# Optimization experiments

Hardware: AMD Instinct MI355X
Metric: run time of the kernel (lower is better)

Reference implementation:

```python
import jax, jax.numpy as jnp
import numpy as np

B, S, D, H = 8, 1024, 1024, 16  # batch, seq (queries==keys), d_model, heads
DH = D // H


def setup_inputs() -> dict:
    key = jax.random.key(0)
    ks = jax.random.split(key, 7)
    return {
        "query": jax.random.normal(ks[0], (B, S, D), dtype=jnp.float32),
        "key": jax.random.normal(ks[1], (B, S, D), dtype=jnp.float32),
        "value": jax.random.normal(ks[2], (B, S, D), dtype=jnp.float32),
        "valid_len": jax.random.randint(ks[3], (B, S), 0, S, dtype=jnp.int32),
        "Wq": jax.random.normal(ks[4], (D, D), dtype=jnp.float32) / np.sqrt(D),
        "Wk": jax.random.normal(ks[5], (D, D), dtype=jnp.float32) / np.sqrt(D),
        "Wv": jax.random.normal(ks[6], (D, D), dtype=jnp.float32) / np.sqrt(D),
    }


def reference(query, key, value, valid_len, Wq, Wk, Wv):
    b, sq, _ = query.shape
    sk = key.shape[1]
    # projections (bias-free Linear), then split hidden into H contiguous chunks per head
    q = (query @ Wq).reshape(b, sq, H, DH)  # [B,Sq,H,dh]
    k = (key @ Wk).reshape(b, sk, H, DH)
    v = (value @ Wv).reshape(b, sk, H, DH)
    scale = 1.0 / jnp.sqrt(jnp.asarray(DH, dtype=q.dtype))
    scores = jnp.einsum("bqhd,bkhd->bhqk", q, k) * scale  # [B,H,Sq,Sk]
    # per-query mask (valid_len.dim()==2 path): key index < valid_len[b, q]
    col = jnp.arange(sk)
    mask = col[None, None, None, :] < valid_len[:, None, :, None]  # [B,1,Sq,Sk]
    scores = jnp.where(mask, scores, jnp.asarray(-1000.0, dtype=scores.dtype))
    prob = jax.nn.softmax(scores, axis=-1)
    out = jnp.einsum("bhqk,bkhd->bqhd", prob, v)  # [B,Sq,H,dh]
    return out.reshape(b, sq, D)
```

## Files before the change

### kernel.cpp

```cpp
#include <hip/hip_runtime.h>
#include <hip/hip_bf16.h>
#include <stdint.h>


#define B_  8
#define S_  1024
#define D_  1024
#define H_  16
#define DH_ 64

typedef short bf16x8 __attribute__((ext_vector_type(8)));
typedef float f32x4  __attribute__((ext_vector_type(4)));
typedef unsigned short u16;
typedef uint32_t u32;
typedef u16 u16x8 __attribute__((ext_vector_type(8)));
typedef u16 u16x4 __attribute__((ext_vector_type(4)));

#define MASKVAL  (-1442.6950408889634f)
#define QSCALE   (0.18033688011112042f)

union U4 { u32 u[4]; bf16x8 v; };

__device__ __forceinline__ u16 f2bf(float f) {
    union { float f; uint32_t u; } v; v.f = f;
    uint32_t u = v.u;
    return (u16)((u + 0x7FFFu + ((u >> 16) & 1u)) >> 16);
}

__device__ __forceinline__ u32 cvtpk(float lo, float hi) {
    u32 r;
    asm("v_cvt_pk_bf16_f32 %0, %1, %2" : "=v"(r) : "v"(lo), "v"(hi));
    return r;
}

__device__ __forceinline__ void gload16(const void* g, const void* l) {
    __builtin_amdgcn_global_load_lds(
        (const __attribute__((address_space(1))) void*)g,
        (__attribute__((address_space(3))) void*)l, 16, 0, 0);
}

__device__ __forceinline__ float xor32max(float v) {
    float a = v, b = v;
    asm volatile("" : "+v"(b));
    asm("v_permlane32_swap_b32 %0, %1" : "+v"(a), "+v"(b));
    return fmaxf(a, b);
}
__device__ __forceinline__ float xor32add(float v) {
    float a = v, b = v;
    asm volatile("" : "+v"(b));
    asm("v_permlane32_swap_b32 %0, %1" : "+v"(a), "+v"(b));
    return a + b;
}

__global__ void transpose_w3_kernel(const float* __restrict__ Wq, const float* __restrict__ Wk,
                                    const float* __restrict__ Wv, u16* __restrict__ Wts) {
    __shared__ u16 tile[32 * 33];
    const int z = blockIdx.z;
    const float* W = (z == 0) ? Wq : (z == 1) ? Wk : Wv;
    u16* Wt = Wts + (size_t)z * D_ * D_;
    int k0 = blockIdx.y * 32, n0 = blockIdx.x * 32;
    int t = threadIdx.x;
    int c = t & 31;
    for (int p = 0; p < 4; ++p) {
        int r = p * 8 + (t >> 5);
        tile[r * 33 + c] = f2bf(W[(size_t)(k0 + r) * D_ + n0 + c]);
    }
    __syncthreads();
    int rn = t >> 3, c4 = t & 7;
    u16x4 v;
    for (int j = 0; j < 4; ++j) v[j] = tile[(c4 * 4 + j) * 33 + rn];
    *(u16x4*)(Wt + (size_t)(n0 + rn) * D_ + k0 + c4 * 4) = v;
}

__global__ __launch_bounds__(1024) void sort_vlen_kernel(const int* __restrict__ vlen,
                                                         int* __restrict__ qidx) {
    __shared__ u32 sk[1024];
    const int b = blockIdx.x, t = threadIdx.x;
    int k = vlen[b * S_ + t];
    u32 key = (k == 0) ? (u32)S_ : (u32)k;
    sk[t] = (key << 10) | (u32)t;
    __syncthreads();
    for (int sz = 2; sz <= 1024; sz <<= 1) {
        for (int st = sz >> 1; st > 0; st >>= 1) {
            int j = t ^ st;
            if (j > t) {
                u32 a = sk[t], c = sk[j];
                bool des = (t & sz) != 0;
                if ((a > c) != des) { sk[t] = c; sk[j] = a; }
            }
            __syncthreads();
        }
    }
    qidx[b * S_ + t] = (int)(sk[t] & 1023u);
}

__global__ __launch_bounds__(512, 4) void gemm_qkv_kernel(const float* __restrict__ Aq,
                                                          const float* __restrict__ Ak,
                                                          const float* __restrict__ Av,
                                                          const u16* __restrict__ wts,
                                                          u16* __restrict__ qb, u16* __restrict__ kb,
                                                          u16* __restrict__ vb) {
    __shared__ float lds_a[2][128 * 32];
    __shared__ u16  lds_b[2][256 * 32];
    const int zy = blockIdx.y;
    const int z = zy >> 2;
    const float* A = (z == 0) ? Aq : (z == 1) ? Ak : Av;
    const u16* Bt = wts + (size_t)z * D_ * D_;
    u16* C = (z == 0) ? qb : (z == 1) ? kb : vb;
    const float cmul = (z == 0) ? QSCALE : 1.0f;

    const int t = threadIdx.x, w = t >> 6, l = t & 63;
    const int m0 = blockIdx.x * 128, n0 = (zy & 3) * 256;
    const int wr = w >> 2, wc = w & 3;
    const int l15 = l & 15, l4 = l >> 4;
    f32x4 acc[4][4] = {};

    auto stage = [&](int buf, int kt) {
        int k0 = kt * 32;
        #pragma unroll
        for (int i = 0; i < 2; ++i) {
            int c = i * 512 + t;
            int row = c >> 3, xs = (c & 7) ^ (row & 7);
            gload16(A + (size_t)(m0 + row) * D_ + k0 + xs * 4, &lds_a[buf][c * 4]);
        }
        #pragma unroll
        for (int i = 0; i < 2; ++i) {
            int c = i * 512 + t;
            int row = c >> 2, x = c & 3;
            gload16(Bt + (size_t)(n0 + row) * D_ + k0 + x * 8, &lds_b[buf][c * 8]);
        }
    };

    stage(0, 0);
    __syncthreads();
    int buf = 0;
    for (int kt = 0; kt < 32; ++kt) {
        if (kt + 1 < 32) stage(buf ^ 1, kt + 1);
        bf16x8 af[4], bfr[4];
        #pragma unroll
        for (int mi = 0; mi < 4; ++mi) {
            int r = wr * 64 + mi * 16 + l15;
            int c0 = (l4 * 2) ^ (r & 7), c1 = (l4 * 2 + 1) ^ (r & 7);
            float4 fa0 = *(const float4*)&lds_a[buf][r * 32 + c0 * 4];
            float4 fa1 = *(const float4*)&lds_a[buf][r * 32 + c1 * 4];
            U4 d;
            d.u[0] = cvtpk(fa0.x, fa0.y); d.u[1] = cvtpk(fa0.z, fa0.w);
            d.u[2] = cvtpk(fa1.x, fa1.y); d.u[3] = cvtpk(fa1.z, fa1.w);
            af[mi] = d.v;
        }
        #pragma unroll
        for (int ni = 0; ni < 4; ++ni) {
            int r = wc * 64 + ni * 16 + l15;
            bfr[ni] = *(const bf16x8*)&lds_b[buf][r * 32 + l4 * 8];
        }
        #pragma unroll
        for (int mi = 0; mi < 4; ++mi)
            #pragma unroll
            for (int ni = 0; ni < 4; ++ni)
                acc[mi][ni] = __builtin_amdgcn_mfma_f32_16x16x32_bf16(af[mi], bfr[ni], acc[mi][ni], 0, 0, 0);
        __syncthreads();
        buf ^= 1;
    }
    #pragma unroll
    for (int mi = 0; mi < 4; ++mi)
        #pragma unroll
        for (int ni = 0; ni < 4; ++ni)
            #pragma unroll
            for (int r = 0; r < 4; ++r) {
                int m = m0 + wr * 64 + mi * 16 + l4 * 4 + r;
                int n = n0 + wc * 64 + ni * 16 + l15;
                C[(size_t)m * D_ + n] = f2bf(acc[mi][ni][r] * cmul);
            }
}

__global__ void transpose_v_kernel(const u16* __restrict__ vb, u16* __restrict__ vt) {
    __shared__ u16 t2[64 * 72];
    int bid = blockIdx.x;
    int st = bid & 15, bh = bid >> 4;
    int b = bh >> 4, h = bh & 15;
    int t = threadIdx.x;
    for (int p = 0; p < 2; ++p) {
        int c = p * 256 + t, r = c >> 3, x = c & 7;
        u16x8 val = *(const u16x8*)&vb[((size_t)(b * S_ + st * 64 + r)) * D_ + h * 64 + x * 8];
        *(u16x8*)&t2[r * 72 + x * 8] = val;
    }
    __syncthreads();
    int d = t >> 2, kc = t & 3;
    u16x8 o0, o1;
    for (int j = 0; j < 8; ++j) o0[j] = t2[(kc * 16 + j) * 72 + d];
    for (int j = 0; j < 8; ++j) o1[j] = t2[(kc * 16 + 8 + j) * 72 + d];
    size_t obase = ((size_t)bh * 64 + d) * (size_t)S_ + st * 64 + kc * 16;
    *(u16x8*)&vt[obase] = o0;
    *(u16x8*)&vt[obase + 8] = o1;
}

__global__ __launch_bounds__(512) void attn_kernel(const u16* __restrict__ qb,
                                                   const u16* __restrict__ kb,
                                                   const u16* __restrict__ vt,
                                                   const int* __restrict__ vlen,
                                                   const int* __restrict__ qidx,
                                                   float* __restrict__ out) {
    __shared__ __align__(16) char smem_raw[34816];
    auto kv = [&](int buf, int which) -> u16* {
        return (u16*)(smem_raw + buf * 16384 + which * 8192);
    };

    const int t = threadIdx.x, w = t >> 6, l = t & 63;
    const int n = blockIdx.x;
    const int x = n & 7, j = n >> 3;
    const int bh = x + 8 * (j >> 2);
    const int p = j & 3;
    const int b = bh >> 4, h = bh & 15;
    const int l15 = l & 15, l4 = l >> 4;
    const bool rowe = ((l & 16) == 0);

    const u16* kbase = kb + ((size_t)(b * S_)) * D_ + h * 64;
    const u16* vbase = vt + ((size_t)bh * 64) * (size_t)S_;

    const int kr_s = t >> 3, x_s = (t & 7) ^ (kr_s & 7);
    auto stage = [&](int buf, int kt) {
        gload16(kbase + (size_t)(kt * 64 + kr_s) * D_ + x_s * 8, &kv(buf, 0)[t * 8]);
        gload16(vbase + (size_t)kr_s * S_ + kt * 64 + x_s * 8, &kv(buf, 1)[t * 8]);
    };

    auto redist = [&](u32 P, u32 Q, u32& oe, u32& oo) {
        u32 X = P, Y = Q;
        asm("v_permlane32_swap_b32 %0, %1" : "+v"(X), "+v"(Y));
        u32 t1 = (u32)__shfl_xor((int)Y, 16, 64);
        u32 t2 = (u32)__shfl_xor((int)X, 16, 64);
        oe = rowe ? X : t1;
        oo = rowe ? t2 : Y;
    };

    auto wavemax = [&](int v) {
        int s1 = __shfl_xor(v, 1, 64);  v = v > s1 ? v : s1;
        int s2 = __shfl_xor(v, 2, 64);  v = v > s2 ? v : s2;
        int s4 = __shfl_xor(v, 4, 64);  v = v > s4 ? v : s4;
        int s8 = __shfl_xor(v, 8, 64);  v = v > s8 ? v : s8;
        return v;
    };

    const int q0a = (7 - p) * 128, q0b = p * 128;

    const int qia = qidx[b * S_ + q0a + w * 16 + l15];
    const u16* qpa = qb + ((size_t)(b * S_ + qia)) * D_ + h * 64 + l4 * 8;
    const bf16x8 bqa0 = *(const bf16x8*)qpa;
    const bf16x8 bqa1 = *(const bf16x8*)(qpa + 32);
    const int vla = vlen[b * S_ + qia];

    const int qib = qidx[b * S_ + q0b + w * 16 + l15];
    const u16* qpb = qb + ((size_t)(b * S_ + qib)) * D_ + h * 64 + l4 * 8;
    const bf16x8 bqb0 = *(const bf16x8*)qpb;
    const bf16x8 bqb1 = *(const bf16x8*)(qpb + 32);
    const int vlb = vlen[b * S_ + qib];

    int mk = vlen[b * S_ + qidx[b * S_ + q0a + 127]];
    if (mk == 0) mk = S_;
    const int nkt = (mk + 63) >> 6;

    const int nktwa = (wavemax(vla == 0 ? S_ : vla) + 63) >> 6;
    const int nktwb = (wavemax(vlb == 0 ? S_ : vlb) + 63) >> 6;

    float ma = -3.0e38f, lsa = 0.f, mb = -3.0e38f, lsb = 0.f;
    f32x4 acca[4] = {}, accb[4] = {};

    auto process = [&](int buf, int kt, const bf16x8& bq0, const bf16x8& bq1, int vlq,
                       float& m, float& lsum, f32x4 (&acc)[4]) {
        f32x4 sc[4];
        __builtin_amdgcn_s_setprio(1);
        #pragma unroll
        for (int nf = 0; nf < 4; ++nf) {
            int kr = nf * 16 + l15, swz = kr & 7;
            bf16x8 ak0 = *(const bf16x8*)&kv(buf, 0)[kr * 64 + ((l4 ^ swz) * 8)];
            bf16x8 ak1 = *(const bf16x8*)&kv(buf, 0)[kr * 64 + (((l4 + 4) ^ swz) * 8)];
            f32x4 s = {0.f, 0.f, 0.f, 0.f};
            s = __builtin_amdgcn_mfma_f32_16x16x32_bf16(ak0, bq0, s, 0, 0, 0);
            s = __builtin_amdgcn_mfma_f32_16x16x32_bf16(ak1, bq1, s, 0, 0, 0);
            sc[nf] = s;
        }
        __builtin_amdgcn_s_setprio(0);

        const int thr = vlq - kt * 64 - 4 * l4;
        float pv[16];
        float pm = -3.0e38f;
        if (__all(thr >= 52)) {
            #pragma unroll
            for (int nf = 0; nf < 4; ++nf)
                #pragma unroll
                for (int r = 0; r < 4; ++r) {
                    float y = sc[nf][r];
                    pv[nf * 4 + r] = y;
                    pm = fmaxf(pm, y);
                }
        } else {
            #pragma unroll
            for (int nf = 0; nf < 4; ++nf)
                #pragma unroll
                for (int r = 0; r < 4; ++r) {
                    float y = ((nf * 16 + r) < thr) ? sc[nf][r] : MASKVAL;
                    pv[nf * 4 + r] = y;
                    pm = fmaxf(pm, y);
                }
        }
        pm = fmaxf(pm, __shfl_xor(pm, 16, 64));
        pm = xor32max(pm);
        if (!__all(pm - m <= 8.0f)) {
            float mn = fmaxf(m, pm);
            float corr = __builtin_amdgcn_exp2f(m - mn);
            m = mn;
            lsum *= corr;
            #pragma unroll
            for (int df = 0; df < 4; ++df) acc[df] *= corr;
        }
        float rs = 0.f;
        #pragma unroll
        for (int i = 0; i < 16; ++i) {
            float e = __builtin_amdgcn_exp2f(pv[i] - m);
            pv[i] = e;
            rs += e;
        }
        rs += __shfl_xor(rs, 16, 64);
        rs = xor32add(rs);
        lsum += rs;

        u32 pw[8];
        #pragma unroll
        for (int nf = 0; nf < 4; ++nf) {
            pw[2 * nf]     = cvtpk(pv[4 * nf + 0], pv[4 * nf + 1]);
            pw[2 * nf + 1] = cvtpk(pv[4 * nf + 2], pv[4 * nf + 3]);
        }
        U4 pb0, pb1;
        redist(pw[0], pw[2], pb0.u[0], pb0.u[2]);
        redist(pw[1], pw[3], pb0.u[1], pb0.u[3]);
        redist(pw[4], pw[6], pb1.u[0], pb1.u[2]);
        redist(pw[5], pw[7], pb1.u[1], pb1.u[3]);

        __builtin_amdgcn_s_setprio(1);
        #pragma unroll
        for (int df = 0; df < 4; ++df) {
            int vr = df * 16 + l15, swz = vr & 7;
            bf16x8 av0 = *(const bf16x8*)&kv(buf, 1)[vr * 64 + ((l4 ^ swz) * 8)];
            bf16x8 av1 = *(const bf16x8*)&kv(buf, 1)[vr * 64 + (((l4 + 4) ^ swz) * 8)];
            acc[df] = __builtin_amdgcn_mfma_f32_16x16x32_bf16(av0, pb0.v, acc[df], 0, 0, 0);
            acc[df] = __builtin_amdgcn_mfma_f32_16x16x32_bf16(av1, pb1.v, acc[df], 0, 0, 0);
        }
        __builtin_amdgcn_s_setprio(0);
    };

    stage(0, 0);
    __syncthreads();

    int buf = 0;
    for (int kt = 0; kt < nkt; ++kt) {
        if (kt + 1 < nkt) stage(buf ^ 1, kt + 1);
        if (kt < nktwa) process(buf, kt, bqa0, bqa1, vla, ma, lsa, acca);
        if (kt < nktwb) process(buf, kt, bqb0, bqb1, vlb, mb, lsb, accb);
        __syncthreads();
        buf ^= 1;
    }

    float* ep = (float*)smem_raw;
    {
        const float inv = 1.0f / lsa;
        #pragma unroll
        for (int df = 0; df < 4; ++df)
            #pragma unroll
            for (int r = 0; r < 4; ++r)
                ep[w * 1088 + l15 * 68 + df * 16 + 4 * l4 + r] = acca[df][r] * inv;
        __syncthreads();
        #pragma unroll
        for (int rr = 0; rr < 4; ++rr) {
            int row = l4 * 4 + rr;
            int qi2 = qidx[b * S_ + q0a + w * 16 + row];
            float4 vv = *(float4*)&ep[w * 1088 + row * 68 + l15 * 4];
            *(float4*)&out[((size_t)(b * S_ + qi2)) * D_ + h * 64 + l15 * 4] = vv;
        }
        __syncthreads();
    }
    {
        const float inv = 1.0f / lsb;
        #pragma unroll
        for (int df = 0; df < 4; ++df)
            #pragma unroll
            for (int r = 0; r < 4; ++r)
                ep[w * 1088 + l15 * 68 + df * 16 + 4 * l4 + r] = accb[df][r] * inv;
        __syncthreads();
        #pragma unroll
        for (int rr = 0; rr < 4; ++rr) {
            int row = l4 * 4 + rr;
            int qi2 = qidx[b * S_ + q0b + w * 16 + row];
            float4 vv = *(float4*)&ep[w * 1088 + row * 68 + l15 * 4];
            *(float4*)&out[((size_t)(b * S_ + qi2)) * D_ + h * 64 + l15 * 4] = vv;
        }
    }
}

extern "C" void kernel_launch(void* const* d_in, const int* in_sizes, int n_in,
                              void* d_out, int out_size, void* d_ws, size_t ws_size,
                              hipStream_t stream) {
    const float* query = (const float*)d_in[0];
    const float* key   = (const float*)d_in[1];
    const float* value = (const float*)d_in[2];
    const int*   vlen  = (const int*)d_in[3];
    const float* Wq    = (const float*)d_in[4];
    const float* Wk    = (const float*)d_in[5];
    const float* Wv    = (const float*)d_in[6];
    float* out = (float*)d_out;

    char* ws = (char*)d_ws;
    const size_t MB = 1024 * 1024;
    const size_t TSZ = (size_t)B_ * S_ * D_ * 2;
    u16* wts = (u16*)(ws);
    u16* vt  = (u16*)(ws + 6 * MB);
    u16* qb  = (u16*)(ws + 6 * MB + TSZ);
    u16* kb  = (u16*)(ws + 6 * MB + 2 * TSZ);
    u16* vb  = (u16*)(ws + 6 * MB + 3 * TSZ);
    int* qidx = (int*)(ws + 6 * MB + 4 * TSZ);

    dim3 blk(256);

    transpose_w3_kernel<<<dim3(32, 32, 3), blk, 0, stream>>>(Wq, Wk, Wv, wts);
    sort_vlen_kernel<<<B_, dim3(1024), 0, stream>>>(vlen, qidx);

    gemm_qkv_kernel<<<dim3(64, 12), dim3(512), 0, stream>>>(query, key, value, wts, qb, kb, vb);

    transpose_v_kernel<<<B_ * H_ * (S_ / 64), blk, 0, stream>>>(vb, vt);

    attn_kernel<<<dim3(512), dim3(512), 0, stream>>>(qb, kb, vt, vlen, qidx, out);
}
```

Measured before the change: 143.5 us.

## Fuse V transpose into QKV GEMM epilogue and drop attention epilogue barriers

```diff
diff --git a/kernel.cpp b/kernel.cpp
--- a/kernel.cpp
+++ b/kernel.cpp
@@ -99,14 +99,15 @@
                                                           const float* __restrict__ Av,
                                                           const u16* __restrict__ wts,
                                                           u16* __restrict__ qb, u16* __restrict__ kb,
-                                                          u16* __restrict__ vb) {
-    __shared__ float lds_a[2][128 * 32];
-    __shared__ u16  lds_b[2][256 * 32];
+                                                          u16* __restrict__ vt) {
+    __shared__ __align__(16) char smem_g[65536];
+    float* lds_a = (float*)smem_g;
+    u16*  lds_b = (u16*)(smem_g + 32768);
     const int zy = blockIdx.y;
     const int z = zy >> 2;
     const float* A = (z == 0) ? Aq : (z == 1) ? Ak : Av;
     const u16* Bt = wts + (size_t)z * D_ * D_;
-    u16* C = (z == 0) ? qb : (z == 1) ? kb : vb;
+    u16* C = (z == 0) ? qb : (z == 1) ? kb : vt;
     const float cmul = (z == 0) ? QSCALE : 1.0f;
 
     const int t = threadIdx.x, w = t >> 6, l = t & 63;
@@ -121,13 +122,13 @@
         for (int i = 0; i < 2; ++i) {
             int c = i * 512 + t;
             int row = c >> 3, xs = (c & 7) ^ (row & 7);
-            gload16(A + (size_t)(m0 + row) * D_ + k0 + xs * 4, &lds_a[buf][c * 4]);
+            gload16(A + (size_t)(m0 + row) * D_ + k0 + xs * 4, &lds_a[buf * 4096 + c * 4]);
         }
         #pragma unroll
         for (int i = 0; i < 2; ++i) {
             int c = i * 512 + t;
             int row = c >> 2, x = c & 3;
-            gload16(Bt + (size_t)(n0 + row) * D_ + k0 + x * 8, &lds_b[buf][c * 8]);
+            gload16(Bt + (size_t)(n0 + row) * D_ + k0 + x * 8, &lds_b[buf * 8192 + c * 8]);
         }
     };
 
@@ -141,8 +142,8 @@
         for (int mi = 0; mi < 4; ++mi) {
             int r = wr * 64 + mi * 16 + l15;
             int c0 = (l4 * 2) ^ (r & 7), c1 = (l4 * 2 + 1) ^ (r & 7);
-            float4 fa0 = *(const float4*)&lds_a[buf][r * 32 + c0 * 4];
-            float4 fa1 = *(const float4*)&lds_a[buf][r * 32 + c1 * 4];
+            float4 fa0 = *(const float4*)&lds_a[buf * 4096 + r * 32 + c0 * 4];
+            float4 fa1 = *(const float4*)&lds_a[buf * 4096 + r * 32 + c1 * 4];
             U4 d;
             d.u[0] = cvtpk(fa0.x, fa0.y); d.u[1] = cvtpk(fa0.z, fa0.w);
             d.u[2] = cvtpk(fa1.x, fa1.y); d.u[3] = cvtpk(fa1.z, fa1.w);
@@ -151,7 +152,7 @@
         #pragma unroll
         for (int ni = 0; ni < 4; ++ni) {
             int r = wc * 64 + ni * 16 + l15;
-            bfr[ni] = *(const bf16x8*)&lds_b[buf][r * 32 + l4 * 8];
+            bfr[ni] = *(const bf16x8*)&lds_b[buf * 8192 + r * 32 + l4 * 8];
         }
         #pragma unroll
         for (int mi = 0; mi < 4; ++mi)
@@ -161,37 +162,40 @@
         __syncthreads();
         buf ^= 1;
     }
-    #pragma unroll
-    for (int mi = 0; mi < 4; ++mi)
-        #pragma unroll
-        for (int ni = 0; ni < 4; ++ni)
-            #pragma unroll
-            for (int r = 0; r < 4; ++r) {
-                int m = m0 + wr * 64 + mi * 16 + l4 * 4 + r;
-                int n = n0 + wc * 64 + ni * 16 + l15;
-                C[(size_t)m * D_ + n] = f2bf(acc[mi][ni][r] * cmul);
-            }
-}
-
-__global__ void transpose_v_kernel(const u16* __restrict__ vb, u16* __restrict__ vt) {
-    __shared__ u16 t2[64 * 72];
-    int bid = blockIdx.x;
-    int st = bid & 15, bh = bid >> 4;
-    int b = bh >> 4, h = bh & 15;
-    int t = threadIdx.x;
-    for (int p = 0; p < 2; ++p) {
-        int c = p * 256 + t, r = c >> 3, x = c & 7;
-        u16x8 val = *(const u16x8*)&vb[((size_t)(b * S_ + st * 64 + r)) * D_ + h * 64 + x * 8];
-        *(u16x8*)&t2[r * 72 + x * 8] = val;
-    }
-    __syncthreads();
-    int d = t >> 2, kc = t & 3;
-    u16x8 o0, o1;
-    for (int j = 0; j < 8; ++j) o0[j] = t2[(kc * 16 + j) * 72 + d];
-    for (int j = 0; j < 8; ++j) o1[j] = t2[(kc * 16 + 8 + j) * 72 + d];
-    size_t obase = ((size_t)bh * 64 + d) * (size_t)S_ + st * 64 + kc * 16;
-    *(u16x8*)&vt[obase] = o0;
-    *(u16x8*)&vt[obase + 8] = o1;
+
+    if (z == 2) {
+        u16* T = (u16*)smem_g;
+        #pragma unroll
+        for (int mi = 0; mi < 4; ++mi)
+            #pragma unroll
+            for (int ni = 0; ni < 4; ++ni)
+                #pragma unroll
+                for (int r = 0; r < 4; ++r) {
+                    int nl = wc * 64 + ni * 16 + l15;
+                    int ml = wr * 64 + mi * 16 + l4 * 4 + r;
+                    T[nl * 128 + (ml ^ ((nl & 7) << 3))] = f2bf(acc[mi][ni][r] * cmul);
+                }
+        __syncthreads();
+        const int nr = t >> 1, hf = t & 1;
+        const size_t vbase = ((size_t)((m0 >> 10) * 1024 + n0 + nr)) * 1024 + (m0 & 1023) + hf * 64;
+        #pragma unroll
+        for (int c = 0; c < 8; ++c) {
+            int cm = hf * 8 + c;
+            u16x8 vv = *(u16x8*)&T[nr * 128 + ((cm ^ (nr & 7)) * 8)];
+            *(u16x8*)&C[vbase + c * 8] = vv;
+        }
+    } else {
+        #pragma unroll
+        for (int mi = 0; mi < 4; ++mi)
+            #pragma unroll
+            for (int ni = 0; ni < 4; ++ni)
+                #pragma unroll
+                for (int r = 0; r < 4; ++r) {
+                    int m = m0 + wr * 64 + mi * 16 + l4 * 4 + r;
+                    int n = n0 + wc * 64 + ni * 16 + l15;
+                    C[(size_t)m * D_ + n] = f2bf(acc[mi][ni][r] * cmul);
+                }
+    }
 }
 
 __global__ __launch_bounds__(512) void attn_kernel(const u16* __restrict__ qb,
@@ -367,7 +371,6 @@
             #pragma unroll
             for (int r = 0; r < 4; ++r)
                 ep[w * 1088 + l15 * 68 + df * 16 + 4 * l4 + r] = acca[df][r] * inv;
-        __syncthreads();
         #pragma unroll
         for (int rr = 0; rr < 4; ++rr) {
             int row = l4 * 4 + rr;
@@ -375,7 +378,6 @@
             float4 vv = *(float4*)&ep[w * 1088 + row * 68 + l15 * 4];
             *(float4*)&out[((size_t)(b * S_ + qi2)) * D_ + h * 64 + l15 * 4] = vv;
         }
-        __syncthreads();
     }
     {
         const float inv = 1.0f / lsb;
@@ -384,7 +386,6 @@
             #pragma unroll
             for (int r = 0; r < 4; ++r)
                 ep[w * 1088 + l15 * 68 + df * 16 + 4 * l4 + r] = accb[df][r] * inv;
-        __syncthreads();
         #pragma unroll
         for (int rr = 0; rr < 4; ++rr) {
             int row = l4 * 4 + rr;
@@ -414,7 +415,6 @@
     u16* vt  = (u16*)(ws + 6 * MB);
     u16* qb  = (u16*)(ws + 6 * MB + TSZ);
     u16* kb  = (u16*)(ws + 6 * MB + 2 * TSZ);
-    u16* vb  = (u16*)(ws + 6 * MB + 3 * TSZ);
     int* qidx = (int*)(ws + 6 * MB + 4 * TSZ);
 
     dim3 blk(256);
@@ -422,9 +422,7 @@
     transpose_w3_kernel<<<dim3(32, 32, 3), blk, 0, stream>>>(Wq, Wk, Wv, wts);
     sort_vlen_kernel<<<B_, dim3(1024), 0, stream>>>(vlen, qidx);
 
-    gemm_qkv_kernel<<<dim3(64, 12), dim3(512), 0, stream>>>(query, key, value, wts, qb, kb, vb);
-
-    transpose_v_kernel<<<B_ * H_ * (S_ / 64), blk, 0, stream>>>(vb, vt);
+    gemm_qkv_kernel<<<dim3(64, 12), dim3(512), 0, stream>>>(query, key, value, wts, qb, kb, vt);
 
     attn_kernel<<<dim3(512), dim3(512), 0, stream>>>(qb, kb, vt, vlen, qidx, out);
 }
```

Measured after the change: 138.5 us (median of 2 runs). 3.5% less time.
